# Optimization experiments

Measured on AMD Instinct MI355X. Metric: run time of the kernel, lower is better.

Reference implementation:

```python
import jax, jax.numpy as jnp
import numpy as np

N, E = 16384, 262144
D_NODE, D_EDGE, H = 256, 64, 8
EPS = 1e-5

def _lin(key, din, dout):
    kw, kb = jax.random.split(key)
    s = 1.0 / np.sqrt(din)
    W = jax.random.uniform(kw, (din, dout), jnp.float32, -s, s)
    b = jax.random.uniform(kb, (dout,), jnp.float32, -s, s)
    return W, b

def setup_inputs() -> dict:
    key = jax.random.key(0)
    ks = jax.random.split(key, 12)
    node_features = jax.random.normal(ks[0], (N, D_NODE), jnp.float32)
    edge_index = jax.random.randint(ks[1], (2, E), 0, N, jnp.int64)
    edge_features = jax.random.normal(ks[2], (E, D_EDGE), jnp.float32)
    Wn, bn = _lin(ks[3], D_NODE, D_NODE)
    Wq, bq = _lin(ks[4], D_NODE, D_NODE)
    Wk, bk = _lin(ks[5], D_NODE, D_NODE)
    Wv, bv = _lin(ks[6], D_NODE, D_NODE)
    We, be = _lin(ks[7], D_EDGE, D_NODE)
    A1, a1 = _lin(ks[8], 3 * D_NODE, D_NODE)
    A2, a2 = _lin(ks[9], D_NODE, H)
    gamma = jnp.ones((D_NODE,), jnp.float32)
    beta = jnp.zeros((D_NODE,), jnp.float32)
    return dict(node_features=node_features, edge_index=edge_index,
                edge_features=edge_features, Wn=Wn, bn=bn, Wq=Wq, bq=bq,
                Wk=Wk, bk=bk, Wv=Wv, bv=bv, We=We, be=be,
                A1=A1, a1=a1, A2=A2, a2=a2, gamma=gamma, beta=beta)

def _leaky(x):
    return jnp.where(x > 0, x, 0.2 * x)

def reference(node_features, edge_index, edge_features, Wn, bn, Wq, bq,
              Wk, bk, Wv, bv, We, be, A1, a1, A2, a2, gamma, beta):
    h = node_features @ Wn + bn                      # [N, d]
    q = node_features @ Wq + bq
    k = node_features @ Wk + bk
    v = node_features @ Wv + bv
    edge_h = edge_features @ We + be                 # [E, d]
    src, tgt = edge_index[0], edge_index[1]
    attn_in = jnp.concatenate([q[src], k[tgt], edge_h], axis=-1)  # [E, 3d]
    scores = _leaky(_leaky(attn_in @ A1 + a1) @ A2 + a2)          # [E, H]
    # softmax over ALL edges (dim=0) of head-mean, as in the original
    w = jax.nn.softmax(scores.mean(axis=-1), axis=0)              # [E]
    out = jnp.zeros_like(node_features).at[src].add(w[:, None] * v[tgt])
    x = h + out                                      # dropout is identity (eval)
    mu = x.mean(-1, keepdims=True)
    var = ((x - mu) ** 2).mean(-1, keepdims=True)
    return (x - mu) / jnp.sqrt(var + EPS) * gamma + beta
```

## Files before the change

### kernel.cpp

```cpp
#include <hip/hip_runtime.h>
#include <stdint.h>

#define NN 16384
#define EE 262144
#define DD 256

typedef float f32x4 __attribute__((ext_vector_type(4)));
typedef short s16x8 __attribute__((ext_vector_type(8)));
typedef unsigned short u16x4 __attribute__((ext_vector_type(4)));
typedef unsigned short u16x8 __attribute__((ext_vector_type(8)));

#define AS1 __attribute__((address_space(1)))
#define AS3 __attribute__((address_space(3)))

__device__ __forceinline__ float bf2f(unsigned short u) {
  union { unsigned int i; float f; } v; v.i = ((unsigned int)u) << 16; return v.f;
}
__device__ __forceinline__ unsigned short f2bf(float f) {
  union { float f; unsigned int i; } v; v.f = f;
  unsigned int r = v.i + 0x7fffu + ((v.i >> 16) & 1u);
  return (unsigned short)(r >> 16);
}
__device__ __forceinline__ float lrelu(float x) { return x > 0.f ? x : 0.2f * x; }

__device__ __forceinline__ int chanperm(int c) {
  int hi = c & ~63, loc = c & 63;
  int ct = loc >> 4, quad = (loc >> 2) & 3, rr = loc & 3;
  return hi | (quad * 16 + ct * 4 + rr);
}

__global__ __launch_bounds__(256) void prep_hist_kernel(
    const float* __restrict__ Wn, const float* __restrict__ bn,
    const float* __restrict__ Wq, const float* __restrict__ bq,
    const float* __restrict__ Wk, const float* __restrict__ bk,
    const float* __restrict__ Wv, const float* __restrict__ bv,
    const float* __restrict__ We, const float* __restrict__ be,
    const float* __restrict__ A1, const float* __restrict__ a1,
    const float* __restrict__ A2, const int* __restrict__ eidx,
    unsigned short* __restrict__ BcatT, float* __restrict__ bcat,
    unsigned short* __restrict__ WeaT, float* __restrict__ bcomb,
    float* __restrict__ A2p, int* __restrict__ deg)
{
  const int b = blockIdx.x, t = threadIdx.x;
  if (b < 256) {
    float acc = 0.f;
    for (int j = 0; j < 256; ++j) acc += Wq[b * 256 + j] * A1[j * 256 + t];
    BcatT[(512 + t) * 256 + b] = f2bf(acc);
  } else if (b < 512) {
    int k = b - 256; float acc = 0.f;
    for (int j = 0; j < 256; ++j) acc += Wk[k * 256 + j] * A1[(256 + j) * 256 + t];
    BcatT[(768 + t) * 256 + k] = f2bf(acc);
  } else if (b < 576) {
    int k = b - 512; float acc = 0.f;
    for (int j = 0; j < 256; ++j) acc += We[k * 256 + j] * A1[(512 + j) * 256 + t];
    WeaT[chanperm(t) * 64 + k] = f2bf(acc);
  } else if (b == 576) {
    float acc = a1[t];
    for (int j = 0; j < 256; ++j) {
      acc += bq[j] * A1[j * 256 + t];
      acc += bk[j] * A1[(256 + j) * 256 + t];
      acc += be[j] * A1[(512 + j) * 256 + t];
    }
    bcomb[chanperm(t)] = acc;
  } else if (b < 705) {
    int b2 = b - 577;
    for (int rr = 0; rr < 4; ++rr) {
      int np = b2 * 4 + rr;
      float v = (np < 256) ? Wn[t * 256 + np] : Wv[t * 256 + (np - 256)];
      BcatT[np * 256 + t] = f2bf(v);
    }
  } else if (b == 705) {
    bcat[t] = bn[t];
    bcat[256 + t] = bv[t];
    bcat[512 + t] = 0.f;
    bcat[768 + t] = 0.f;
  } else if (b == 706) {
    int m = chanperm(t);
    for (int j = 0; j < 8; ++j) A2p[m * 8 + j] = A2[t * 8 + j];
  } else {
    int e = (b - 707) * 256 + t;
    atomicAdd(&deg[eidx[e]], 1);
  }
}

__global__ __launch_bounds__(256) void conv_scan_kernel(
    const float* __restrict__ in, unsigned short* __restrict__ o,
    const int* __restrict__ deg, int* __restrict__ startA,
    int* __restrict__ cursor)
{
  const int t = threadIdx.x;
  if (blockIdx.x < 2048) {
    size_t i = (size_t)blockIdx.x * 256 + t;
    const f32x4* p = (const f32x4*)(in + i * 8);
    f32x4 a = p[0], b = p[1];
    u16x8 r = { f2bf(a[0]), f2bf(a[1]), f2bf(a[2]), f2bf(a[3]),
                f2bf(b[0]), f2bf(b[1]), f2bf(b[2]), f2bf(b[3]) };
    *(u16x8*)(o + i * 8) = r;
    return;
  }
  __shared__ int ls[256];
  int4 d[16];
  int s = 0;
  #pragma unroll
  for (int i = 0; i < 16; ++i) {
    d[i] = ((const int4*)deg)[t * 16 + i];
    s += d[i].x + d[i].y + d[i].z + d[i].w;
  }
  ls[t] = s;
  __syncthreads();
  for (int dd = 1; dd < 256; dd <<= 1) {
    int v = ls[t];
    if (t >= dd) v += ls[t - dd];
    __syncthreads();
    ls[t] = v;
    __syncthreads();
  }
  int run = ls[t] - s;
  #pragma unroll
  for (int i = 0; i < 16; ++i) {
    int4 ov;
    ov.x = run; run += d[i].x;
    ov.y = run; run += d[i].y;
    ov.z = run; run += d[i].z;
    ov.w = run; run += d[i].w;
    ((int4*)startA)[t * 16 + i] = ov;
    ((int4*)cursor)[t * 16 + i] = ov;
  }
  if (t == 255) startA[NN] = run;
}

__global__ __launch_bounds__(256, 1) void gemm_perm_kernel(
    const unsigned short* __restrict__ Abf,
    const unsigned short* __restrict__ BT,
    const float* __restrict__ bias,
    unsigned short* __restrict__ hout, unsigned short* __restrict__ vout,
    unsigned short* __restrict__ Qa, unsigned short* __restrict__ Ka,
    const int* __restrict__ eidx, int* __restrict__ cursor,
    int* __restrict__ perm, int* __restrict__ srcp, int* __restrict__ tgtp)
{
  const int t = threadIdx.x;
  if (blockIdx.x < 1024) {
    int e = blockIdx.x * 256 + t;
    int s = eidx[e], tg = eidx[EE + e];
    int pos = atomicAdd(&cursor[s], 1);
    perm[pos] = e;
    srcp[pos] = s;
    tgtp[pos] = tg;
    return;
  }
  __shared__ __align__(16) unsigned short Al[128 * 64];
  __shared__ __align__(16) unsigned short Bl[128 * 64];
  const int b2 = blockIdx.x - 1024;
  const int wid = t >> 6, lane = t & 63;
  const int quad = lane >> 4, l15 = lane & 15;
  const int mblk = b2 & 127, nblk = b2 >> 7;
  const int m0 = mblk * 128, n0 = nblk * 128;
  const int mh = wid >> 1, nh = wid & 1;
  const int srow = lane >> 3, sslot = lane & 7;

  f32x4 acc[4][4];
  #pragma unroll
  for (int i = 0; i < 4; ++i)
    #pragma unroll
    for (int j = 0; j < 4; ++j) acc[i][j] = (f32x4){0.f, 0.f, 0.f, 0.f};

  for (int ks = 0; ks < 4; ++ks) {
    const int k0 = ks * 64;
    #pragma unroll
    for (int j = 0; j < 4; ++j) {
      int cj = wid * 4 + j;
      int row = cj * 8 + srow;
      const unsigned short* ga =
          Abf + (size_t)(m0 + row) * 256 + k0 + ((sslot ^ (row & 7)) * 8);
      __builtin_amdgcn_global_load_lds((AS1 const void*)ga,
                                       (AS3 void*)(Al + cj * 512), 16, 0, 0);
      const unsigned short* gb =
          BT + (size_t)(n0 + row) * 256 + k0 + ((sslot ^ (row & 7)) * 8);
      __builtin_amdgcn_global_load_lds((AS1 const void*)gb,
                                       (AS3 void*)(Bl + cj * 512), 16, 0, 0);
    }
    __syncthreads();
    s16x8 af[4][2], bfr[4][2];
    #pragma unroll
    for (int mt = 0; mt < 4; ++mt) {
      int row = mh * 64 + mt * 16 + l15;
      #pragma unroll
      for (int kk = 0; kk < 2; ++kk) {
        int s = (kk * 4 + quad) ^ (row & 7);
        af[mt][kk] = *(const s16x8*)(Al + row * 64 + s * 8);
      }
    }
    #pragma unroll
    for (int nt = 0; nt < 4; ++nt) {
      int row = nh * 64 + nt * 16 + l15;
      #pragma unroll
      for (int kk = 0; kk < 2; ++kk) {
        int s = (kk * 4 + quad) ^ (row & 7);
        bfr[nt][kk] = *(const s16x8*)(Bl + row * 64 + s * 8);
      }
    }
    #pragma unroll
    for (int mt = 0; mt < 4; ++mt)
      #pragma unroll
      for (int nt = 0; nt < 4; ++nt) {
        acc[mt][nt] = __builtin_amdgcn_mfma_f32_16x16x32_bf16(
            af[mt][0], bfr[nt][0], acc[mt][nt], 0, 0, 0);
        acc[mt][nt] = __builtin_amdgcn_mfma_f32_16x16x32_bf16(
            af[mt][1], bfr[nt][1], acc[mt][nt], 0, 0, 0);
      }
    __syncthreads();
  }

  #pragma unroll
  for (int nt = 0; nt < 4; ++nt) {
    int n = n0 + nh * 64 + nt * 16 + l15;
    float bb = bias[n];
    int seg = n >> 8;
    int ncol = n & 255;
    #pragma unroll
    for (int mt = 0; mt < 4; ++mt) {
      int m = m0 + mh * 64 + mt * 16 + quad * 4;
      f32x4 a = acc[mt][nt];
      #pragma unroll
      for (int r = 0; r < 4; ++r) {
        float val = a[r] + bb;
        size_t idx = (size_t)(m + r) * 256 + ncol;
        if (seg == 0) hout[idx] = f2bf(val);
        else if (seg == 1) vout[idx] = f2bf(val);
        else if (seg == 2) Qa[idx] = f2bf(val);
        else Ka[idx] = f2bf(val);
      }
    }
  }
}

__global__ __launch_bounds__(256, 4) void edge_scores_kernel(
    const int* __restrict__ perm, const int* __restrict__ srcp,
    const int* __restrict__ tgtp, const float* __restrict__ ef,
    const unsigned short* __restrict__ Qa, const unsigned short* __restrict__ Ka,
    const unsigned short* __restrict__ WeaT, const float* __restrict__ bcomb,
    const float* __restrict__ A2p, const float* __restrict__ a2g,
    float* __restrict__ Pp, float* __restrict__ Zpart)
{
  __shared__ __align__(16) unsigned short efl[64 * 64];
  __shared__ __align__(16) float A2l[256 * 12];
  __shared__ __align__(16) float pl[4 * 64 * 8];
  __shared__ __align__(16) float bcl[256];
  __shared__ int srcl[64], tgtl[64];
  const int t = threadIdx.x;
  const int wid = t >> 6, lane = t & 63, quad = lane >> 4, l15 = lane & 15;
  const int base = blockIdx.x * 256;
  const int r = t >> 2, q4 = t & 3;

  {
    const f32x4* sp = (const f32x4*)(A2p + t * 8);
    f32x4 x0 = sp[0], x1 = sp[1];
    *(f32x4*)&A2l[t * 12] = x0;
    *(f32x4*)&A2l[t * 12 + 4] = x1;
  }
  if (t < 64) ((f32x4*)bcl)[t] = ((const f32x4*)bcomb)[t];

  s16x8 af0[4], af1[4];
  #pragma unroll
  for (int ct = 0; ct < 4; ++ct) {
    int ch = wid * 64 + ct * 16 + l15;
    af0[ct] = *(const s16x8*)(WeaT + ch * 64 + quad * 8);
    af1[ct] = *(const s16x8*)(WeaT + ch * 64 + 32 + quad * 8);
  }
  const f32x4 a20 = *(const f32x4*)a2g;
  const f32x4 a21 = *(const f32x4*)(a2g + 4);

  int pe = perm[base + r];
  int rs = (t < 128) ? ((t < 64) ? srcp[base + t] : tgtp[base + t - 64]) : 0;
  f32x4 v0, v1, v2, v3;
  {
    const f32x4* sp = (const f32x4*)(ef + (size_t)pe * 64 + q4 * 16);
    v0 = sp[0]; v1 = sp[1]; v2 = sp[2]; v3 = sp[3];
  }
  int pe_n = perm[base + 64 + r];

  float zacc = 0.f;

  #pragma unroll
  for (int k = 0; k < 4; ++k) {
    const int eb = base + k * 64;
    {
      u16x8 w0 = { f2bf(v0[0]), f2bf(v0[1]), f2bf(v0[2]), f2bf(v0[3]),
                   f2bf(v1[0]), f2bf(v1[1]), f2bf(v1[2]), f2bf(v1[3]) };
      u16x8 w1 = { f2bf(v2[0]), f2bf(v2[1]), f2bf(v2[2]), f2bf(v2[3]),
                   f2bf(v3[0]), f2bf(v3[1]), f2bf(v3[2]), f2bf(v3[3]) };
      int s0_ = (2 * q4) ^ (r & 7), s1_ = (2 * q4 + 1) ^ (r & 7);
      *(u16x8*)&efl[r * 64 + s0_ * 8] = w0;
      *(u16x8*)&efl[r * 64 + s1_ * 8] = w1;
    }
    if (t < 64) srcl[t] = rs;
    else if (t < 128) tgtl[t - 64] = rs;
    if (k < 3) {
      rs = (t < 128) ? ((t < 64) ? srcp[eb + 64 + t] : tgtp[eb + t]) : 0;
      const f32x4* sp = (const f32x4*)(ef + (size_t)pe_n * 64 + q4 * 16);
      v0 = sp[0]; v1 = sp[1]; v2 = sp[2]; v3 = sp[3];
      if (k < 2) pe_n = perm[eb + 128 + r];
    }
    __syncthreads();

    f32x4 acc[4][4];
    {
      const int cb = wid * 64 + quad * 16;
      #pragma unroll
      for (int eo = 0; eo < 2; ++eo) {
        u16x8 q0[2], q1[2], k0[2], k1[2];
        #pragma unroll
        for (int x = 0; x < 2; ++x) {
          int e = (eo * 2 + x) * 16 + l15;
          const unsigned short* qr = Qa + (size_t)srcl[e] * 256 + cb;
          const unsigned short* kr = Ka + (size_t)tgtl[e] * 256 + cb;
          q0[x] = *(const u16x8*)qr; q1[x] = *(const u16x8*)(qr + 8);
          k0[x] = *(const u16x8*)kr; k1[x] = *(const u16x8*)(kr + 8);
        }
        #pragma unroll
        for (int x = 0; x < 2; ++x) {
          int et = eo * 2 + x;
          #pragma unroll
          for (int rr = 0; rr < 4; ++rr) {
            acc[0][et][rr] = bf2f(q0[x][rr])     + bf2f(k0[x][rr]);
            acc[1][et][rr] = bf2f(q0[x][4 + rr]) + bf2f(k0[x][4 + rr]);
            acc[2][et][rr] = bf2f(q1[x][rr])     + bf2f(k1[x][rr]);
            acc[3][et][rr] = bf2f(q1[x][4 + rr]) + bf2f(k1[x][4 + rr]);
          }
        }
      }
    }
    #pragma unroll
    for (int et = 0; et < 4; ++et) {
      int e = et * 16 + l15;
      s16x8 b0 = *(const s16x8*)(efl + e * 64 + ((quad ^ (e & 7)) * 8));
      s16x8 b1 = *(const s16x8*)(efl + e * 64 + (((4 + quad) ^ (e & 7)) * 8));
      #pragma unroll
      for (int ct = 0; ct < 4; ++ct) {
        acc[ct][et] = __builtin_amdgcn_mfma_f32_16x16x32_bf16(af0[ct], b0, acc[ct][et], 0, 0, 0);
        acc[ct][et] = __builtin_amdgcn_mfma_f32_16x16x32_bf16(af1[ct], b1, acc[ct][et], 0, 0, 0);
      }
    }
    float part[4][8];
    #pragma unroll
    for (int i = 0; i < 4; ++i)
      #pragma unroll
      for (int j = 0; j < 8; ++j) part[i][j] = 0.f;
    #pragma unroll
    for (int ct = 0; ct < 4; ++ct) {
      int chb = wid * 64 + ct * 16 + quad * 4;
      f32x4 bc = *(const f32x4*)&bcl[chb];
      #pragma unroll
      for (int rr = 0; rr < 4; ++rr) {
        f32x4 w0 = *(const f32x4*)&A2l[(chb + rr) * 12];
        f32x4 w1 = *(const f32x4*)&A2l[(chb + rr) * 12 + 4];
        #pragma unroll
        for (int et = 0; et < 4; ++et) {
          float m = lrelu(acc[ct][et][rr] + bc[rr]);
          part[et][0] += m * w0[0]; part[et][1] += m * w0[1];
          part[et][2] += m * w0[2]; part[et][3] += m * w0[3];
          part[et][4] += m * w1[0]; part[et][5] += m * w1[1];
          part[et][6] += m * w1[2]; part[et][7] += m * w1[3];
        }
      }
    }
    #pragma unroll
    for (int et = 0; et < 4; ++et)
      #pragma unroll
      for (int hh = 0; hh < 8; ++hh) {
        part[et][hh] += __shfl_xor(part[et][hh], 16);
        part[et][hh] += __shfl_xor(part[et][hh], 32);
      }
    if (quad == 0) {
      #pragma unroll
      for (int et = 0; et < 4; ++et) {
        f32x4 p0 = { part[et][0], part[et][1], part[et][2], part[et][3] };
        f32x4 p1 = { part[et][4], part[et][5], part[et][6], part[et][7] };
        int e = et * 16 + l15;
        *(f32x4*)&pl[(wid * 64 + e) * 8] = p0;
        *(f32x4*)&pl[(wid * 64 + e) * 8 + 4] = p1;
      }
    }
    __syncthreads();
    if (t < 64) {
      f32x4 t0 = {0.f, 0.f, 0.f, 0.f}, t1 = {0.f, 0.f, 0.f, 0.f};
      #pragma unroll
      for (int w2 = 0; w2 < 4; ++w2) {
        t0 += *(const f32x4*)&pl[(w2 * 64 + t) * 8];
        t1 += *(const f32x4*)&pl[(w2 * 64 + t) * 8 + 4];
      }
      float sacc = 0.f;
      #pragma unroll
      for (int j = 0; j < 4; ++j) {
        sacc += lrelu(t0[j] + a20[j]);
        sacc += lrelu(t1[j] + a21[j]);
      }
      float p = __expf(sacc * 0.125f);
      Pp[eb + t] = p;
      #pragma unroll
      for (int d = 1; d < 64; d <<= 1) p += __shfl_xor(p, d);
      zacc += p;
    }
  }
  if (t == 0) atomicAdd(&Zpart[blockIdx.x & 63], zacc);
}

__global__ __launch_bounds__(256) void scatter_ln_kernel(
    const int* __restrict__ startA, const float* __restrict__ Pp,
    const float* __restrict__ Zpart, const int* __restrict__ tgtp,
    const unsigned short* __restrict__ vbuf, const unsigned short* __restrict__ hbuf,
    const float* __restrict__ gamma, const float* __restrict__ beta,
    float* __restrict__ out)
{
  const int wid = threadIdx.x >> 6, lane = threadIdx.x & 63;
  const int n = blockIdx.x * 4 + wid;
  float zv = Zpart[lane];
  #pragma unroll
  for (int d = 1; d < 64; d <<= 1) zv += __shfl_xor(zv, d);
  const float invZ = 1.f / zv;
  const int s0 = startA[n], s1 = startA[n + 1];
  float a0 = 0.f, a1_ = 0.f, a2_ = 0.f, a3_ = 0.f;
  int i = s0;
  for (; i + 3 < s1; i += 4) {
    float w0 = Pp[i], w1 = Pp[i + 1], w2 = Pp[i + 2], w3 = Pp[i + 3];
    int t0 = tgtp[i], t1 = tgtp[i + 1], t2 = tgtp[i + 2], t3 = tgtp[i + 3];
    u16x4 e0 = *(const u16x4*)(vbuf + (size_t)t0 * 256 + lane * 4);
    u16x4 e1 = *(const u16x4*)(vbuf + (size_t)t1 * 256 + lane * 4);
    u16x4 e2 = *(const u16x4*)(vbuf + (size_t)t2 * 256 + lane * 4);
    u16x4 e3 = *(const u16x4*)(vbuf + (size_t)t3 * 256 + lane * 4);
    w0 *= invZ; w1 *= invZ; w2 *= invZ; w3 *= invZ;
    a0 += w0 * bf2f(e0[0]) + w1 * bf2f(e1[0]) + w2 * bf2f(e2[0]) + w3 * bf2f(e3[0]);
    a1_ += w0 * bf2f(e0[1]) + w1 * bf2f(e1[1]) + w2 * bf2f(e2[1]) + w3 * bf2f(e3[1]);
    a2_ += w0 * bf2f(e0[2]) + w1 * bf2f(e1[2]) + w2 * bf2f(e2[2]) + w3 * bf2f(e3[2]);
    a3_ += w0 * bf2f(e0[3]) + w1 * bf2f(e1[3]) + w2 * bf2f(e2[3]) + w3 * bf2f(e3[3]);
  }
  for (; i < s1; ++i) {
    float w0 = Pp[i] * invZ;
    int t0 = tgtp[i];
    u16x4 e0 = *(const u16x4*)(vbuf + (size_t)t0 * 256 + lane * 4);
    a0 += w0 * bf2f(e0[0]); a1_ += w0 * bf2f(e0[1]);
    a2_ += w0 * bf2f(e0[2]); a3_ += w0 * bf2f(e0[3]);
  }
  u16x4 hv = *(const u16x4*)(hbuf + (size_t)n * 256 + lane * 4);
  float x0 = bf2f(hv[0]) + a0, x1 = bf2f(hv[1]) + a1_;
  float x2 = bf2f(hv[2]) + a2_, x3 = bf2f(hv[3]) + a3_;
  float sum = x0 + x1 + x2 + x3;
  float sq = x0 * x0 + x1 * x1 + x2 * x2 + x3 * x3;
  #pragma unroll
  for (int d = 1; d < 64; d <<= 1) { sum += __shfl_xor(sum, d); sq += __shfl_xor(sq, d); }
  float mu = sum * (1.f / 256.f);
  float var = sq * (1.f / 256.f) - mu * mu;
  float rstd = rsqrtf(var + 1e-5f);
  f32x4 g = *(const f32x4*)(gamma + lane * 4);
  f32x4 b = *(const f32x4*)(beta + lane * 4);
  f32x4 o;
  o[0] = (x0 - mu) * rstd * g[0] + b[0];
  o[1] = (x1 - mu) * rstd * g[1] + b[1];
  o[2] = (x2 - mu) * rstd * g[2] + b[2];
  o[3] = (x3 - mu) * rstd * g[3] + b[3];
  *(f32x4*)(out + (size_t)n * 256 + lane * 4) = o;
}

extern "C" void kernel_launch(void* const* d_in, const int* in_sizes, int n_in,
                              void* d_out, int out_size, void* d_ws, size_t ws_size,
                              hipStream_t stream)
{
  (void)in_sizes; (void)n_in; (void)out_size; (void)ws_size;
  const float* nf    = (const float*)d_in[0];
  const int*   eidx  = (const int*)  d_in[1];
  const float* ef    = (const float*)d_in[2];
  const float* Wn    = (const float*)d_in[3];
  const float* bn    = (const float*)d_in[4];
  const float* Wq    = (const float*)d_in[5];
  const float* bq    = (const float*)d_in[6];
  const float* Wk    = (const float*)d_in[7];
  const float* bk    = (const float*)d_in[8];
  const float* Wv    = (const float*)d_in[9];
  const float* bv    = (const float*)d_in[10];
  const float* We    = (const float*)d_in[11];
  const float* be    = (const float*)d_in[12];
  const float* A1    = (const float*)d_in[13];
  const float* a1    = (const float*)d_in[14];
  const float* A2    = (const float*)d_in[15];
  const float* a2    = (const float*)d_in[16];
  const float* gamma = (const float*)d_in[17];
  const float* beta  = (const float*)d_in[18];
  float* out = (float*)d_out;

  char* ws = (char*)d_ws;
  size_t off = 0;
  auto take = [&](size_t bytes) {
    size_t r = off; off += (bytes + 255) & ~(size_t)255; return r;
  };
  float* Zpart   = (float*)(ws + take(256));
  int*   deg     = (int*)  (ws + take((size_t)NN * 4));
  int*   startA  = (int*)  (ws + take((size_t)(NN + 1) * 4));
  int*   cursor  = (int*)  (ws + take((size_t)NN * 4));
  int*   perm    = (int*)  (ws + take((size_t)EE * 4));
  int*   srcp    = (int*)  (ws + take((size_t)EE * 4));
  int*   tgtp    = (int*)  (ws + take((size_t)EE * 4));
  float* Pp      = (float*)(ws + take((size_t)EE * 4));
  unsigned short* hbuf  = (unsigned short*)(ws + take((size_t)NN * DD * 2));
  unsigned short* vbuf  = (unsigned short*)(ws + take((size_t)NN * DD * 2));
  unsigned short* QaB   = (unsigned short*)(ws + take((size_t)NN * DD * 2));
  unsigned short* KaB   = (unsigned short*)(ws + take((size_t)NN * DD * 2));
  unsigned short* BcatT = (unsigned short*)(ws + take((size_t)1024 * 256 * 2));
  float* bcat    = (float*)(ws + take(1024 * 4));
  unsigned short* WeaT  = (unsigned short*)(ws + take((size_t)256 * 64 * 2));
  float* bcomb   = (float*)(ws + take(256 * 4));
  float* A2p     = (float*)(ws + take(256 * 8 * 4));
  unsigned short* nfb   = (unsigned short*)(ws + take((size_t)NN * DD * 2));

  hipMemsetAsync(d_ws, 0, 256 + (size_t)NN * 4, stream);

  prep_hist_kernel<<<1731, 256, 0, stream>>>(Wn, bn, Wq, bq, Wk, bk, Wv, bv,
                                             We, be, A1, a1, A2, eidx,
                                             BcatT, bcat, WeaT, bcomb, A2p, deg);
  conv_scan_kernel<<<2049, 256, 0, stream>>>(nf, nfb, deg, startA, cursor);
  gemm_perm_kernel<<<2048, 256, 0, stream>>>(nfb, BcatT, bcat, hbuf, vbuf,
                                             QaB, KaB, eidx, cursor,
                                             perm, srcp, tgtp);
  edge_scores_kernel<<<1024, 256, 0, stream>>>(perm, srcp, tgtp, ef, QaB, KaB,
                                               WeaT, bcomb, A2p, a2, Pp, Zpart);
  scatter_ln_kernel<<<NN / 4, 256, 0, stream>>>(startA, Pp, Zpart, tgtp,
                                                vbuf, hbuf, gamma, beta, out);
}
```

Measured before the change: 350.5 us.

## Store Q, K, V projections in FP8 and split edge-score blocks to one tile

```diff
diff --git a/kernel.cpp b/kernel.cpp
--- a/kernel.cpp
+++ b/kernel.cpp
@@ -6,6 +6,7 @@
 #define DD 256
 
 typedef float f32x4 __attribute__((ext_vector_type(4)));
+typedef float f32x2 __attribute__((ext_vector_type(2)));
 typedef short s16x8 __attribute__((ext_vector_type(8)));
 typedef unsigned short u16x4 __attribute__((ext_vector_type(4)));
 typedef unsigned short u16x8 __attribute__((ext_vector_type(8)));
@@ -22,6 +23,44 @@
   return (unsigned short)(r >> 16);
 }
 __device__ __forceinline__ float lrelu(float x) { return x > 0.f ? x : 0.2f * x; }
+
+__device__ __forceinline__ uint8_t f2e4m3(float x) {
+  uint32_t xu = __float_as_uint(x);
+  uint32_t s = (xu >> 24) & 0x80u;
+  float a = fabsf(x);
+  if (a >= 448.f) return (uint8_t)(s | 0x7Eu);
+  if (a < 0.015625f) return (uint8_t)s;
+  uint32_t u = xu & 0x7FFFFFFFu;
+  u = u + 0x0007FFFFu + ((u >> 20) & 1u);
+  uint32_t E = (u >> 23) - 120u;
+  if (E >= 16u) return (uint8_t)(s | 0x7Eu);
+  return (uint8_t)(s | (E << 3) | ((u >> 20) & 7u));
+}
+__device__ __forceinline__ float e4m3f(uint32_t b) {
+  uint32_t ex = b & 0x78u;
+  uint32_t bits = ((b & 0x80u) << 24) | (((b & 0x7fu) << 20) + (120u << 23));
+  union { uint32_t u; float f; } v;
+  v.u = ex ? bits : ((b & 0x80u) << 24);
+  return v.f;
+}
+#if defined(__has_builtin)
+#if __has_builtin(__builtin_amdgcn_cvt_pk_f32_fp8)
+#define HAVE_CVT_FP8 1
+#endif
+#endif
+__device__ __forceinline__ void dec4(uint32_t w, float* f) {
+#ifdef HAVE_CVT_FP8
+  f32x2 lo = __builtin_amdgcn_cvt_pk_f32_fp8(w, false);
+  f32x2 hi = __builtin_amdgcn_cvt_pk_f32_fp8(w, true);
+  f[0] = lo[0]; f[1] = lo[1]; f[2] = hi[0]; f[3] = hi[1];
+#else
+  f[0] = e4m3f(w & 0xFFu); f[1] = e4m3f((w >> 8) & 0xFFu);
+  f[2] = e4m3f((w >> 16) & 0xFFu); f[3] = e4m3f(w >> 24);
+#endif
+}
+__device__ __forceinline__ void dec16(uint4 v, float* f) {
+  dec4(v.x, f); dec4(v.y, f + 4); dec4(v.z, f + 8); dec4(v.w, f + 12);
+}
 
 __device__ __forceinline__ int chanperm(int c) {
   int hi = c & ~63, loc = c & 63;
@@ -133,8 +172,8 @@
     const unsigned short* __restrict__ Abf,
     const unsigned short* __restrict__ BT,
     const float* __restrict__ bias,
-    unsigned short* __restrict__ hout, unsigned short* __restrict__ vout,
-    unsigned short* __restrict__ Qa, unsigned short* __restrict__ Ka,
+    unsigned short* __restrict__ hout, uint8_t* __restrict__ vq,
+    uint8_t* __restrict__ Qaq, uint8_t* __restrict__ Kaq,
     const int* __restrict__ eidx, int* __restrict__ cursor,
     int* __restrict__ perm, int* __restrict__ srcp, int* __restrict__ tgtp)
 {
@@ -226,9 +265,9 @@
         float val = a[r] + bb;
         size_t idx = (size_t)(m + r) * 256 + ncol;
         if (seg == 0) hout[idx] = f2bf(val);
-        else if (seg == 1) vout[idx] = f2bf(val);
-        else if (seg == 2) Qa[idx] = f2bf(val);
-        else Ka[idx] = f2bf(val);
+        else if (seg == 1) vq[idx] = f2e4m3(val);
+        else if (seg == 2) Qaq[idx] = f2e4m3(val);
+        else Kaq[idx] = f2e4m3(val);
       }
     }
   }
@@ -237,29 +276,46 @@
 __global__ __launch_bounds__(256, 4) void edge_scores_kernel(
     const int* __restrict__ perm, const int* __restrict__ srcp,
     const int* __restrict__ tgtp, const float* __restrict__ ef,
-    const unsigned short* __restrict__ Qa, const unsigned short* __restrict__ Ka,
+    const uint8_t* __restrict__ Qaq, const uint8_t* __restrict__ Kaq,
     const unsigned short* __restrict__ WeaT, const float* __restrict__ bcomb,
     const float* __restrict__ A2p, const float* __restrict__ a2g,
     float* __restrict__ Pp, float* __restrict__ Zpart)
 {
   __shared__ __align__(16) unsigned short efl[64 * 64];
-  __shared__ __align__(16) float A2l[256 * 12];
+  __shared__ __align__(16) float A2l[8][260];
   __shared__ __align__(16) float pl[4 * 64 * 8];
   __shared__ __align__(16) float bcl[256];
   __shared__ int srcl[64], tgtl[64];
   const int t = threadIdx.x;
   const int wid = t >> 6, lane = t & 63, quad = lane >> 4, l15 = lane & 15;
-  const int base = blockIdx.x * 256;
+  const int wg = ((blockIdx.x & 7) << 9) | (blockIdx.x >> 3);
+  const int eb = wg * 64;
   const int r = t >> 2, q4 = t & 3;
 
   {
-    const f32x4* sp = (const f32x4*)(A2p + t * 8);
-    f32x4 x0 = sp[0], x1 = sp[1];
-    *(f32x4*)&A2l[t * 12] = x0;
-    *(f32x4*)&A2l[t * 12 + 4] = x1;
+    const f32x4 x0 = *(const f32x4*)(A2p + t * 8);
+    const f32x4 x1 = *(const f32x4*)(A2p + t * 8 + 4);
+    A2l[0][t] = x0[0]; A2l[1][t] = x0[1]; A2l[2][t] = x0[2]; A2l[3][t] = x0[3];
+    A2l[4][t] = x1[0]; A2l[5][t] = x1[1]; A2l[6][t] = x1[2]; A2l[7][t] = x1[3];
   }
   if (t < 64) ((f32x4*)bcl)[t] = ((const f32x4*)bcomb)[t];
-
+  else if (t < 128) srcl[t - 64] = srcp[eb + (t - 64)];
+  else if (t < 192) tgtl[t - 128] = tgtp[eb + (t - 128)];
+  {
+    int pe = __builtin_nontemporal_load(&perm[eb + r]);
+    const f32x4* sp = (const f32x4*)(ef + (size_t)pe * 64 + q4 * 16);
+    f32x4 v0 = __builtin_nontemporal_load(sp);
+    f32x4 v1 = __builtin_nontemporal_load(sp + 1);
+    f32x4 v2 = __builtin_nontemporal_load(sp + 2);
+    f32x4 v3 = __builtin_nontemporal_load(sp + 3);
+    u16x8 w0 = { f2bf(v0[0]), f2bf(v0[1]), f2bf(v0[2]), f2bf(v0[3]),
+                 f2bf(v1[0]), f2bf(v1[1]), f2bf(v1[2]), f2bf(v1[3]) };
+    u16x8 w1 = { f2bf(v2[0]), f2bf(v2[1]), f2bf(v2[2]), f2bf(v2[3]),
+                 f2bf(v3[0]), f2bf(v3[1]), f2bf(v3[2]), f2bf(v3[3]) };
+    int s0_ = (2 * q4) ^ (r & 7), s1_ = (2 * q4 + 1) ^ (r & 7);
+    *(u16x8*)&efl[r * 64 + s0_ * 8] = w0;
+    *(u16x8*)&efl[r * 64 + s1_ * 8] = w1;
+  }
   s16x8 af0[4], af1[4];
   #pragma unroll
   for (int ct = 0; ct < 4; ++ct) {
@@ -267,148 +323,111 @@
     af0[ct] = *(const s16x8*)(WeaT + ch * 64 + quad * 8);
     af1[ct] = *(const s16x8*)(WeaT + ch * 64 + 32 + quad * 8);
   }
-  const f32x4 a20 = *(const f32x4*)a2g;
-  const f32x4 a21 = *(const f32x4*)(a2g + 4);
-
-  int pe = perm[base + r];
-  int rs = (t < 128) ? ((t < 64) ? srcp[base + t] : tgtp[base + t - 64]) : 0;
-  f32x4 v0, v1, v2, v3;
+  __syncthreads();
+
+  f32x4 acc[4][4];
   {
-    const f32x4* sp = (const f32x4*)(ef + (size_t)pe * 64 + q4 * 16);
-    v0 = sp[0]; v1 = sp[1]; v2 = sp[2]; v3 = sp[3];
-  }
-  int pe_n = perm[base + 64 + r];
-
-  float zacc = 0.f;
-
-  #pragma unroll
-  for (int k = 0; k < 4; ++k) {
-    const int eb = base + k * 64;
-    {
-      u16x8 w0 = { f2bf(v0[0]), f2bf(v0[1]), f2bf(v0[2]), f2bf(v0[3]),
-                   f2bf(v1[0]), f2bf(v1[1]), f2bf(v1[2]), f2bf(v1[3]) };
-      u16x8 w1 = { f2bf(v2[0]), f2bf(v2[1]), f2bf(v2[2]), f2bf(v2[3]),
-                   f2bf(v3[0]), f2bf(v3[1]), f2bf(v3[2]), f2bf(v3[3]) };
-      int s0_ = (2 * q4) ^ (r & 7), s1_ = (2 * q4 + 1) ^ (r & 7);
-      *(u16x8*)&efl[r * 64 + s0_ * 8] = w0;
-      *(u16x8*)&efl[r * 64 + s1_ * 8] = w1;
-    }
-    if (t < 64) srcl[t] = rs;
-    else if (t < 128) tgtl[t - 64] = rs;
-    if (k < 3) {
-      rs = (t < 128) ? ((t < 64) ? srcp[eb + 64 + t] : tgtp[eb + t]) : 0;
-      const f32x4* sp = (const f32x4*)(ef + (size_t)pe_n * 64 + q4 * 16);
-      v0 = sp[0]; v1 = sp[1]; v2 = sp[2]; v3 = sp[3];
-      if (k < 2) pe_n = perm[eb + 128 + r];
-    }
-    __syncthreads();
-
-    f32x4 acc[4][4];
-    {
-      const int cb = wid * 64 + quad * 16;
-      #pragma unroll
-      for (int eo = 0; eo < 2; ++eo) {
-        u16x8 q0[2], q1[2], k0[2], k1[2];
+    const int cb = wid * 64 + quad * 16;
+    uint4 qv[4], kv[4];
+    #pragma unroll
+    for (int x = 0; x < 4; ++x) {
+      int e = x * 16 + l15;
+      qv[x] = *(const uint4*)(Qaq + (size_t)srcl[e] * 256 + cb);
+      kv[x] = *(const uint4*)(Kaq + (size_t)tgtl[e] * 256 + cb);
+    }
+    #pragma unroll
+    for (int x = 0; x < 4; ++x) {
+      float qf[16], kf[16];
+      dec16(qv[x], qf); dec16(kv[x], kf);
+      #pragma unroll
+      for (int ct = 0; ct < 4; ++ct)
         #pragma unroll
-        for (int x = 0; x < 2; ++x) {
-          int e = (eo * 2 + x) * 16 + l15;
-          const unsigned short* qr = Qa + (size_t)srcl[e] * 256 + cb;
-          const unsigned short* kr = Ka + (size_t)tgtl[e] * 256 + cb;
-          q0[x] = *(const u16x8*)qr; q1[x] = *(const u16x8*)(qr + 8);
-          k0[x] = *(const u16x8*)kr; k1[x] = *(const u16x8*)(kr + 8);
-        }
-        #pragma unroll
-        for (int x = 0; x < 2; ++x) {
-          int et = eo * 2 + x;
-          #pragma unroll
-          for (int rr = 0; rr < 4; ++rr) {
-            acc[0][et][rr] = bf2f(q0[x][rr])     + bf2f(k0[x][rr]);
-            acc[1][et][rr] = bf2f(q0[x][4 + rr]) + bf2f(k0[x][4 + rr]);
-            acc[2][et][rr] = bf2f(q1[x][rr])     + bf2f(k1[x][rr]);
-            acc[3][et][rr] = bf2f(q1[x][4 + rr]) + bf2f(k1[x][4 + rr]);
-          }
-        }
-      }
-    }
+        for (int rr = 0; rr < 4; ++rr)
+          acc[ct][x][rr] = qf[ct * 4 + rr] + kf[ct * 4 + rr];
+    }
+  }
+
+  #pragma unroll
+  for (int et = 0; et < 4; ++et) {
+    int e = et * 16 + l15;
+    s16x8 b0 = *(const s16x8*)(efl + e * 64 + ((quad ^ (e & 7)) * 8));
+    s16x8 b1 = *(const s16x8*)(efl + e * 64 + (((4 + quad) ^ (e & 7)) * 8));
+    #pragma unroll
+    for (int ct = 0; ct < 4; ++ct) {
+      acc[ct][et] = __builtin_amdgcn_mfma_f32_16x16x32_bf16(af0[ct], b0, acc[ct][et], 0, 0, 0);
+      acc[ct][et] = __builtin_amdgcn_mfma_f32_16x16x32_bf16(af1[ct], b1, acc[ct][et], 0, 0, 0);
+    }
+  }
+
+  float part[4][8];
+  #pragma unroll
+  for (int i = 0; i < 4; ++i)
+    #pragma unroll
+    for (int j = 0; j < 8; ++j) part[i][j] = 0.f;
+  #pragma unroll
+  for (int ct = 0; ct < 4; ++ct) {
+    int chb = wid * 64 + ct * 16 + quad * 4;
+    f32x4 bc = *(const f32x4*)&bcl[chb];
+    float mv[4][4];
+    #pragma unroll
+    for (int et = 0; et < 4; ++et)
+      #pragma unroll
+      for (int rr = 0; rr < 4; ++rr)
+        mv[et][rr] = lrelu(acc[ct][et][rr] + bc[rr]);
+    #pragma unroll
+    for (int hh = 0; hh < 8; ++hh) {
+      f32x4 w = *(const f32x4*)&A2l[hh][chb];
+      #pragma unroll
+      for (int et = 0; et < 4; ++et)
+        part[et][hh] += mv[et][0] * w[0] + mv[et][1] * w[1] +
+                        mv[et][2] * w[2] + mv[et][3] * w[3];
+    }
+  }
+  #pragma unroll
+  for (int et = 0; et < 4; ++et)
+    #pragma unroll
+    for (int hh = 0; hh < 8; ++hh) {
+      part[et][hh] += __shfl_xor(part[et][hh], 16);
+      part[et][hh] += __shfl_xor(part[et][hh], 32);
+    }
+  if (quad == 0) {
     #pragma unroll
     for (int et = 0; et < 4; ++et) {
+      f32x4 p0 = { part[et][0], part[et][1], part[et][2], part[et][3] };
+      f32x4 p1 = { part[et][4], part[et][5], part[et][6], part[et][7] };
       int e = et * 16 + l15;
-      s16x8 b0 = *(const s16x8*)(efl + e * 64 + ((quad ^ (e & 7)) * 8));
-      s16x8 b1 = *(const s16x8*)(efl + e * 64 + (((4 + quad) ^ (e & 7)) * 8));
-      #pragma unroll
-      for (int ct = 0; ct < 4; ++ct) {
-        acc[ct][et] = __builtin_amdgcn_mfma_f32_16x16x32_bf16(af0[ct], b0, acc[ct][et], 0, 0, 0);
-        acc[ct][et] = __builtin_amdgcn_mfma_f32_16x16x32_bf16(af1[ct], b1, acc[ct][et], 0, 0, 0);
-      }
-    }
-    float part[4][8];
-    #pragma unroll
-    for (int i = 0; i < 4; ++i)
-      #pragma unroll
-      for (int j = 0; j < 8; ++j) part[i][j] = 0.f;
-    #pragma unroll
-    for (int ct = 0; ct < 4; ++ct) {
-      int chb = wid * 64 + ct * 16 + quad * 4;
-      f32x4 bc = *(const f32x4*)&bcl[chb];
-      #pragma unroll
-      for (int rr = 0; rr < 4; ++rr) {
-        f32x4 w0 = *(const f32x4*)&A2l[(chb + rr) * 12];
-        f32x4 w1 = *(const f32x4*)&A2l[(chb + rr) * 12 + 4];
-        #pragma unroll
-        for (int et = 0; et < 4; ++et) {
-          float m = lrelu(acc[ct][et][rr] + bc[rr]);
-          part[et][0] += m * w0[0]; part[et][1] += m * w0[1];
-          part[et][2] += m * w0[2]; part[et][3] += m * w0[3];
-          part[et][4] += m * w1[0]; part[et][5] += m * w1[1];
-          part[et][6] += m * w1[2]; part[et][7] += m * w1[3];
-        }
-      }
-    }
-    #pragma unroll
-    for (int et = 0; et < 4; ++et)
-      #pragma unroll
-      for (int hh = 0; hh < 8; ++hh) {
-        part[et][hh] += __shfl_xor(part[et][hh], 16);
-        part[et][hh] += __shfl_xor(part[et][hh], 32);
-      }
-    if (quad == 0) {
-      #pragma unroll
-      for (int et = 0; et < 4; ++et) {
-        f32x4 p0 = { part[et][0], part[et][1], part[et][2], part[et][3] };
-        f32x4 p1 = { part[et][4], part[et][5], part[et][6], part[et][7] };
-        int e = et * 16 + l15;
-        *(f32x4*)&pl[(wid * 64 + e) * 8] = p0;
-        *(f32x4*)&pl[(wid * 64 + e) * 8 + 4] = p1;
-      }
-    }
-    __syncthreads();
-    if (t < 64) {
-      f32x4 t0 = {0.f, 0.f, 0.f, 0.f}, t1 = {0.f, 0.f, 0.f, 0.f};
-      #pragma unroll
-      for (int w2 = 0; w2 < 4; ++w2) {
-        t0 += *(const f32x4*)&pl[(w2 * 64 + t) * 8];
-        t1 += *(const f32x4*)&pl[(w2 * 64 + t) * 8 + 4];
-      }
-      float sacc = 0.f;
-      #pragma unroll
-      for (int j = 0; j < 4; ++j) {
-        sacc += lrelu(t0[j] + a20[j]);
-        sacc += lrelu(t1[j] + a21[j]);
-      }
-      float p = __expf(sacc * 0.125f);
-      Pp[eb + t] = p;
-      #pragma unroll
-      for (int d = 1; d < 64; d <<= 1) p += __shfl_xor(p, d);
-      zacc += p;
-    }
-  }
-  if (t == 0) atomicAdd(&Zpart[blockIdx.x & 63], zacc);
+      *(f32x4*)&pl[(wid * 64 + e) * 8] = p0;
+      *(f32x4*)&pl[(wid * 64 + e) * 8 + 4] = p1;
+    }
+  }
+  __syncthreads();
+  if (t < 64) {
+    f32x4 t0 = {0.f, 0.f, 0.f, 0.f}, t1 = {0.f, 0.f, 0.f, 0.f};
+    #pragma unroll
+    for (int w2 = 0; w2 < 4; ++w2) {
+      t0 += *(const f32x4*)&pl[(w2 * 64 + t) * 8];
+      t1 += *(const f32x4*)&pl[(w2 * 64 + t) * 8 + 4];
+    }
+    const f32x4 a20 = *(const f32x4*)a2g;
+    const f32x4 a21 = *(const f32x4*)(a2g + 4);
+    float sacc = 0.f;
+    #pragma unroll
+    for (int j = 0; j < 4; ++j) {
+      sacc += lrelu(t0[j] + a20[j]);
+      sacc += lrelu(t1[j] + a21[j]);
+    }
+    float p = __expf(sacc * 0.125f);
+    Pp[eb + t] = p;
+    #pragma unroll
+    for (int d = 1; d < 64; d <<= 1) p += __shfl_xor(p, d);
+    if (t == 0) atomicAdd(&Zpart[wg & 63], p);
+  }
 }
 
 __global__ __launch_bounds__(256) void scatter_ln_kernel(
     const int* __restrict__ startA, const float* __restrict__ Pp,
     const float* __restrict__ Zpart, const int* __restrict__ tgtp,
-    const unsigned short* __restrict__ vbuf, const unsigned short* __restrict__ hbuf,
+    const uint8_t* __restrict__ vq, const unsigned short* __restrict__ hbuf,
     const float* __restrict__ gamma, const float* __restrict__ beta,
     float* __restrict__ out)
 {
@@ -424,24 +443,27 @@
   for (; i + 3 < s1; i += 4) {
     float w0 = Pp[i], w1 = Pp[i + 1], w2 = Pp[i + 2], w3 = Pp[i + 3];
     int t0 = tgtp[i], t1 = tgtp[i + 1], t2 = tgtp[i + 2], t3 = tgtp[i + 3];
-    u16x4 e0 = *(const u16x4*)(vbuf + (size_t)t0 * 256 + lane * 4);
-    u16x4 e1 = *(const u16x4*)(vbuf + (size_t)t1 * 256 + lane * 4);
-    u16x4 e2 = *(const u16x4*)(vbuf + (size_t)t2 * 256 + lane * 4);
-    u16x4 e3 = *(const u16x4*)(vbuf + (size_t)t3 * 256 + lane * 4);
-    w0 *= invZ; w1 *= invZ; w2 *= invZ; w3 *= invZ;
-    a0 += w0 * bf2f(e0[0]) + w1 * bf2f(e1[0]) + w2 * bf2f(e2[0]) + w3 * bf2f(e3[0]);
-    a1_ += w0 * bf2f(e0[1]) + w1 * bf2f(e1[1]) + w2 * bf2f(e2[1]) + w3 * bf2f(e3[1]);
-    a2_ += w0 * bf2f(e0[2]) + w1 * bf2f(e1[2]) + w2 * bf2f(e2[2]) + w3 * bf2f(e3[2]);
-    a3_ += w0 * bf2f(e0[3]) + w1 * bf2f(e1[3]) + w2 * bf2f(e2[3]) + w3 * bf2f(e3[3]);
+    uint32_t e0 = *(const uint32_t*)(vq + (size_t)t0 * 256 + lane * 4);
+    uint32_t e1 = *(const uint32_t*)(vq + (size_t)t1 * 256 + lane * 4);
+    uint32_t e2 = *(const uint32_t*)(vq + (size_t)t2 * 256 + lane * 4);
+    uint32_t e3 = *(const uint32_t*)(vq + (size_t)t3 * 256 + lane * 4);
+    float f0[4], f1[4], f2[4], f3[4];
+    dec4(e0, f0); dec4(e1, f1); dec4(e2, f2); dec4(e3, f3);
+    a0 += w0 * f0[0] + w1 * f1[0] + w2 * f2[0] + w3 * f3[0];
+    a1_ += w0 * f0[1] + w1 * f1[1] + w2 * f2[1] + w3 * f3[1];
+    a2_ += w0 * f0[2] + w1 * f1[2] + w2 * f2[2] + w3 * f3[2];
+    a3_ += w0 * f0[3] + w1 * f1[3] + w2 * f2[3] + w3 * f3[3];
   }
   for (; i < s1; ++i) {
-    float w0 = Pp[i] * invZ;
-    int t0 = tgtp[i];
-    u16x4 e0 = *(const u16x4*)(vbuf + (size_t)t0 * 256 + lane * 4);
-    a0 += w0 * bf2f(e0[0]); a1_ += w0 * bf2f(e0[1]);
-    a2_ += w0 * bf2f(e0[2]); a3_ += w0 * bf2f(e0[3]);
-  }
-  u16x4 hv = *(const u16x4*)(hbuf + (size_t)n * 256 + lane * 4);
+    float w0 = Pp[i];
+    uint32_t e0 = *(const uint32_t*)(vq + (size_t)tgtp[i] * 256 + lane * 4);
+    float f0[4];
+    dec4(e0, f0);
+    a0 += w0 * f0[0]; a1_ += w0 * f0[1]; a2_ += w0 * f0[2]; a3_ += w0 * f0[3];
+  }
+  a0 *= invZ; a1_ *= invZ; a2_ *= invZ; a3_ *= invZ;
+  u16x4 hv = __builtin_nontemporal_load(
+      (const u16x4*)(hbuf + (size_t)n * 256 + lane * 4));
   float x0 = bf2f(hv[0]) + a0, x1 = bf2f(hv[1]) + a1_;
   float x2 = bf2f(hv[2]) + a2_, x3 = bf2f(hv[3]) + a3_;
   float sum = x0 + x1 + x2 + x3;
@@ -500,10 +522,10 @@
   int*   srcp    = (int*)  (ws + take((size_t)EE * 4));
   int*   tgtp    = (int*)  (ws + take((size_t)EE * 4));
   float* Pp      = (float*)(ws + take((size_t)EE * 4));
-  unsigned short* hbuf  = (unsigned short*)(ws + take((size_t)NN * DD * 2));
-  unsigned short* vbuf  = (unsigned short*)(ws + take((size_t)NN * DD * 2));
-  unsigned short* QaB   = (unsigned short*)(ws + take((size_t)NN * DD * 2));
-  unsigned short* KaB   = (unsigned short*)(ws + take((size_t)NN * DD * 2));
+  unsigned short* hbuf = (unsigned short*)(ws + take((size_t)NN * DD * 2));
+  uint8_t* vqB   = (uint8_t*)(ws + take((size_t)NN * DD));
+  uint8_t* QaB   = (uint8_t*)(ws + take((size_t)NN * DD));
+  uint8_t* KaB   = (uint8_t*)(ws + take((size_t)NN * DD));
   unsigned short* BcatT = (unsigned short*)(ws + take((size_t)1024 * 256 * 2));
   float* bcat    = (float*)(ws + take(1024 * 4));
   unsigned short* WeaT  = (unsigned short*)(ws + take((size_t)256 * 64 * 2));
@@ -517,11 +539,11 @@
                                              We, be, A1, a1, A2, eidx,
                                              BcatT, bcat, WeaT, bcomb, A2p, deg);
   conv_scan_kernel<<<2049, 256, 0, stream>>>(nf, nfb, deg, startA, cursor);
-  gemm_perm_kernel<<<2048, 256, 0, stream>>>(nfb, BcatT, bcat, hbuf, vbuf,
+  gemm_perm_kernel<<<2048, 256, 0, stream>>>(nfb, BcatT, bcat, hbuf, vqB,
                                              QaB, KaB, eidx, cursor,
                                              perm, srcp, tgtp);
-  edge_scores_kernel<<<1024, 256, 0, stream>>>(perm, srcp, tgtp, ef, QaB, KaB,
+  edge_scores_kernel<<<4096, 256, 0, stream>>>(perm, srcp, tgtp, ef, QaB, KaB,
                                                WeaT, bcomb, A2p, a2, Pp, Zpart);
   scatter_ln_kernel<<<NN / 4, 256, 0, stream>>>(startA, Pp, Zpart, tgtp,
-                                                vbuf, hbuf, gamma, beta, out);
-}
+                                                vqB, hbuf, gamma, beta, out);
+}
```

Result: no change. 343.8 us (-1.9%).
